# Performance work log

Hardware: AMD Instinct MI355X
Metric: run time of the kernel (lower is better)

The kernel has to match this reference:

```python
import jax, jax.numpy as jnp
import numpy as np

N, E, G = 100000, 600000, 2000
CONV = [128, 256, 256, 256]
LIN = [256, 128, 1]
BN_EPS = 1e-5


def setup_inputs() -> dict:
    key = jax.random.key(0)
    ks = iter(jax.random.split(key, 64))
    inp = {}
    inp["x"] = jax.random.normal(next(ks), (N, CONV[0]), dtype=jnp.float32)
    inp["edge_index"] = jax.random.randint(next(ks), (2, E), 0, N)
    inp["batch"] = jnp.sort(jax.random.randint(next(ks), (N,), 0, G))

    def lin_w(k, i, o):
        return (jax.random.normal(k, (i, o), dtype=jnp.float32) / np.sqrt(i)).astype(jnp.float32)

    # 3 GINConv MLPs: Linear(in,out), BN(out), ReLU, Linear(out,out), ReLU
    for i in range(3):
        ci, co = CONV[i], CONV[i + 1]
        inp[f"c{i}_w1"] = lin_w(next(ks), ci, co)
        inp[f"c{i}_b1"] = jnp.zeros((co,), jnp.float32)
        inp[f"c{i}_g"] = jnp.ones((co,), jnp.float32)
        inp[f"c{i}_be"] = jnp.zeros((co,), jnp.float32)
        inp[f"c{i}_m"] = jax.random.normal(next(ks), (co,), dtype=jnp.float32) * 0.1
        inp[f"c{i}_v"] = jax.random.uniform(next(ks), (co,), minval=0.5, maxval=1.5, dtype=jnp.float32)
        inp[f"c{i}_w2"] = lin_w(next(ks), co, co)
        inp[f"c{i}_b2"] = jnp.zeros((co,), jnp.float32)
    # head: Linear(256,128) + BN(128) + ReLU, Linear(128,1)
    inp["l0_w"] = lin_w(next(ks), LIN[0], LIN[1])
    inp["l0_b"] = jnp.zeros((LIN[1],), jnp.float32)
    inp["l0_g"] = jnp.ones((LIN[1],), jnp.float32)
    inp["l0_be"] = jnp.zeros((LIN[1],), jnp.float32)
    inp["l0_m"] = jax.random.normal(next(ks), (LIN[1],), dtype=jnp.float32) * 0.1
    inp["l0_v"] = jax.random.uniform(next(ks), (LIN[1],), minval=0.5, maxval=1.5, dtype=jnp.float32)
    inp["l1_w"] = lin_w(next(ks), LIN[1], LIN[2])
    inp["l1_b"] = jnp.zeros((LIN[2],), jnp.float32)
    return inp


def _bn(h, g, be, m, v):
    return g * (h - m) * jax.lax.rsqrt(v + BN_EPS) + be


def _gin_conv(x, src, dst, w1, b1, g, be, m, v, w2, b2):
    # GINConv (eps=0): MLP(x + sum_{j in N(i)} x_j); messages x[src] aggregated at dst
    agg = jax.ops.segment_sum(x[src], dst, num_segments=x.shape[0])
    h = (x + agg) @ w1 + b1
    h = jax.nn.relu(_bn(h, g, be, m, v))
    return jax.nn.relu(h @ w2 + b2)


def reference(x, edge_index, batch,
              c0_w1, c0_b1, c0_g, c0_be, c0_m, c0_v, c0_w2, c0_b2,
              c1_w1, c1_b1, c1_g, c1_be, c1_m, c1_v, c1_w2, c1_b2,
              c2_w1, c2_b1, c2_g, c2_be, c2_m, c2_v, c2_w2, c2_b2,
              l0_w, l0_b, l0_g, l0_be, l0_m, l0_v, l1_w, l1_b):
    src, dst = edge_index[0], edge_index[1]
    conv_params = [
        (c0_w1, c0_b1, c0_g, c0_be, c0_m, c0_v, c0_w2, c0_b2),
        (c1_w1, c1_b1, c1_g, c1_be, c1_m, c1_v, c1_w2, c1_b2),
        (c2_w1, c2_b1, c2_g, c2_be, c2_m, c2_v, c2_w2, c2_b2),
    ]
    h = x
    for i, p in enumerate(conv_params):
        h = _gin_conv(h, src, dst, *p)
        if i < 2:
            h = jax.nn.relu(h)  # outer activation (no-op after ReLU, kept for fidelity)
    # global_add_pool over graphs
    h = jax.ops.segment_sum(h, batch, num_segments=G)  # [G, 256]
    h = h @ l0_w + l0_b
    h = _bn(h, l0_g, l0_be, l0_m, l0_v)
    h = jax.nn.relu(h)  # dropout is identity in eval mode
    return h @ l1_w + l1_b  # [G, 1]
```

## Files before the change

kernel.cpp:

```cpp
#include <hip/hip_runtime.h>
#include <hip/hip_bf16.h>

#define BN_EPS 1e-5f

typedef __attribute__((ext_vector_type(8))) short short8;
typedef __attribute__((ext_vector_type(4))) float f32x4;

__device__ __forceinline__ void gll16(const void* g, void* l) {
    __builtin_amdgcn_global_load_lds(
        (const __attribute__((address_space(1))) unsigned int*)g,
        (__attribute__((address_space(3))) unsigned int*)l, 16, 0, 0);
}

__device__ __forceinline__ unsigned pack_bf2(float a, float b) {
    __hip_bfloat16 ba = __float2bfloat16(a);
    __hip_bfloat16 bb = __float2bfloat16(b);
    return (unsigned)(*(unsigned short*)&ba) | ((unsigned)(*(unsigned short*)&bb) << 16);
}

__global__ void hist_kernel(const int* __restrict__ dst, int* __restrict__ off, int E) {
    int e = blockIdx.x * blockDim.x + threadIdx.x;
    if (e < E) atomicAdd(&off[dst[e] + 1], 1);
}

__global__ __launch_bounds__(256) void scan1_kernel(int* __restrict__ data,
                                                    int* __restrict__ sums, int n) {
    __shared__ int sh[256];
    const int t = threadIdx.x;
    const int idx = blockIdx.x * 1024 + t * 4;
    int v[4];
    int s = 0;
#pragma unroll
    for (int j = 0; j < 4; ++j) {
        int x = (idx + j < n) ? data[idx + j] : 0;
        s += x;
        v[j] = s;
    }
    sh[t] = s;
    __syncthreads();
    for (int o = 1; o < 256; o <<= 1) {
        int x = (t >= o) ? sh[t - o] : 0;
        __syncthreads();
        sh[t] += x;
        __syncthreads();
    }
    const int prev = sh[t] - s;
#pragma unroll
    for (int j = 0; j < 4; ++j) {
        if (idx + j < n) data[idx + j] = v[j] + prev;
    }
    if (t == 255) sums[blockIdx.x] = sh[255];
}

__global__ __launch_bounds__(256) void scan2_kernel(int* __restrict__ sums, int nb) {
    __shared__ int sh[256];
    const int t = threadIdx.x;
    sh[t] = (t < nb) ? sums[t] : 0;
    __syncthreads();
    for (int o = 1; o < 256; o <<= 1) {
        int x = (t >= o) ? sh[t - o] : 0;
        __syncthreads();
        sh[t] += x;
        __syncthreads();
    }
    if (t < nb) sums[t] = sh[t];
}

__global__ void scan3_kernel(int* __restrict__ data, const int* __restrict__ sums,
                             int* __restrict__ cursor, int n, int N) {
    int i = blockIdx.x * blockDim.x + threadIdx.x;
    if (i >= n) return;
    int b = i >> 10;
    int v = data[i];
    if (b > 0) { v += sums[b - 1]; data[i] = v; }
    if (i < N) cursor[i] = v;
}

__global__ void fill_kernel(const int* __restrict__ src, const int* __restrict__ dst,
                            int* __restrict__ cursor, int* __restrict__ sorted_src, int E) {
    int e = blockIdx.x * blockDim.x + threadIdx.x;
    if (e >= E) return;
    int p = atomicAdd(&cursor[dst[e]], 1);
    sorted_src[p] = src[e];
}

__global__ void cvt_x_kernel(const float* __restrict__ x, __hip_bfloat16* __restrict__ xb,
                             int N, int total ) {
    int i = blockIdx.x * blockDim.x + threadIdx.x;
    if (i >= total) return;
    int n = i >> 7;
    float v = (n < N) ? x[i] : 0.f;
    xb[i] = __float2bfloat16(v);
}

__global__ void wt_all_kernel(const float* __restrict__ w0, const float* __restrict__ w1,
                              const float* __restrict__ w2, const float* __restrict__ w3,
                              const float* __restrict__ w4, const float* __restrict__ w5,
                              __hip_bfloat16* __restrict__ o0, __hip_bfloat16* __restrict__ o1,
                              __hip_bfloat16* __restrict__ o2, __hip_bfloat16* __restrict__ o3,
                              __hip_bfloat16* __restrict__ o4, __hip_bfloat16* __restrict__ o5) {
    int i = blockIdx.x * blockDim.x + threadIdx.x;
    const int S0 = 256 * 128, S = 256 * 256;
    if (i < S0) {
        int m = i / 128, k = i - m * 128;
        o0[i] = __float2bfloat16(w0[k * 256 + m]);
        return;
    }
    i -= S0;
    int mi = i / S, j = i - mi * S;
    if (mi >= 5) return;
    int m = j >> 8, k = j & 255;
    const float* Wp; __hip_bfloat16* Op;
    switch (mi) {
        case 0: Wp = w1; Op = o1; break;
        case 1: Wp = w2; Op = o2; break;
        case 2: Wp = w3; Op = o3; break;
        case 3: Wp = w4; Op = o4; break;
        default: Wp = w5; Op = o5; break;
    }
    Op[j] = __float2bfloat16(Wp[k * 256 + m]);
}

__global__ void prep_ss_kernel(
    const float* __restrict__ g0, const float* __restrict__ be0, const float* __restrict__ m0,
    const float* __restrict__ v0, const float* __restrict__ b10, const float* __restrict__ b20,
    const float* __restrict__ g1, const float* __restrict__ be1, const float* __restrict__ m1,
    const float* __restrict__ v1, const float* __restrict__ b11, const float* __restrict__ b21,
    const float* __restrict__ g2, const float* __restrict__ be2, const float* __restrict__ m2,
    const float* __restrict__ v2, const float* __restrict__ b12, const float* __restrict__ b22,
    float* __restrict__ ss) {
    const int layer = blockIdx.x;
    const int c = threadIdx.x;
    const float *g, *be, *m, *v, *b1, *b2;
    switch (layer) {
        case 0: g = g0; be = be0; m = m0; v = v0; b1 = b10; b2 = b20; break;
        case 1: g = g1; be = be1; m = m1; v = v1; b1 = b11; b2 = b21; break;
        default: g = g2; be = be2; m = m2; v = v2; b1 = b12; b2 = b22; break;
    }
    float r = rsqrtf(v[c] + BN_EPS);
    float s = g[c] * r;
    ss[(2 * layer) * 512 + c] = s;
    ss[(2 * layer) * 512 + 256 + c] = (b1[c] - m[c]) * s + be[c];
    ss[(2 * layer + 1) * 512 + c] = 1.f;
    ss[(2 * layer + 1) * 512 + 256 + c] = b2[c];
}

template <int C>
__global__ __launch_bounds__(256) void agg_fused(const __hip_bfloat16* __restrict__ h,
                                                 const int* __restrict__ off,
                                                 const int* __restrict__ ssrc,
                                                 __hip_bfloat16* __restrict__ out, int N) {
    constexpr int L = C / 8;
    int t = blockIdx.x * blockDim.x + threadIdx.x;
    int n = t / L;
    if (n >= N) return;
    int c8 = t - n * L;
    const uint4* hp = (const uint4*)h;

    float acc[8];
    {
        uint4 sv = hp[(size_t)n * L + c8];
        const unsigned u[4] = {sv.x, sv.y, sv.z, sv.w};
#pragma unroll
        for (int j = 0; j < 4; ++j) {
            acc[2 * j]     = __uint_as_float(u[j] << 16);
            acc[2 * j + 1] = __uint_as_float(u[j] & 0xffff0000u);
        }
    }
    const int e0 = off[n], e1 = off[n + 1];
    int e = e0;
    for (; e + 2 <= e1; e += 2) {
        int s0 = ssrc[e], s1 = ssrc[e + 1];
        uint4 a = hp[(size_t)s0 * L + c8];
        uint4 b = hp[(size_t)s1 * L + c8];
        const unsigned ua[4] = {a.x, a.y, a.z, a.w};
        const unsigned ub[4] = {b.x, b.y, b.z, b.w};
#pragma unroll
        for (int j = 0; j < 4; ++j) {
            acc[2 * j]     += __uint_as_float(ua[j] << 16);
            acc[2 * j + 1] += __uint_as_float(ua[j] & 0xffff0000u);
            acc[2 * j]     += __uint_as_float(ub[j] << 16);
            acc[2 * j + 1] += __uint_as_float(ub[j] & 0xffff0000u);
        }
    }
    if (e < e1) {
        int s0 = ssrc[e];
        uint4 a = hp[(size_t)s0 * L + c8];
        const unsigned ua[4] = {a.x, a.y, a.z, a.w};
#pragma unroll
        for (int j = 0; j < 4; ++j) {
            acc[2 * j]     += __uint_as_float(ua[j] << 16);
            acc[2 * j + 1] += __uint_as_float(ua[j] & 0xffff0000u);
        }
    }
    unsigned o[4];
#pragma unroll
    for (int j = 0; j < 4; ++j) o[j] = pack_bf2(acc[2 * j], acc[2 * j + 1]);
    ((uint4*)out)[(size_t)n * L + c8] = make_uint4(o[0], o[1], o[2], o[3]);
}

template <int K1>
__global__ __launch_bounds__(512) void mlp_fused(
    const __hip_bfloat16* __restrict__ A,
    const __hip_bfloat16* __restrict__ W1t,
    const __hip_bfloat16* __restrict__ W2t,
    const float* __restrict__ ss1, const float* __restrict__ ss2,
    __hip_bfloat16* __restrict__ C) {
    __shared__ __align__(16) char bufAT[64 * 1024];
    __shared__ __align__(16) char bufW[2][32 * 1024];

    const int tid = threadIdx.x;
    const int l   = tid & 63;
    const int w   = tid >> 6;
    const int wr  = w >> 2;
    const int wc  = w & 3;
    const size_t row0 = (size_t)blockIdx.x * 128;

    constexpr int ROWB = K1 * 2;
    constexpr int NT1  = K1 / 64;
    constexpr int NIA  = 128 * ROWB / 1024;
    constexpr int RPI  = 1024 / ROWB;

    const int lswz = (l & 7) << 4;

    {
        const char* Ab = (const char*)(A + row0 * K1);
#pragma unroll
        for (int i = w; i < NIA; i += 8) {
            int row = i * RPI + (l * 16) / ROWB;
            int byt = ((l * 16) % ROWB) ^ ((row & 7) << 4);
            gll16(Ab + (size_t)row * ROWB + byt, bufAT + i * 1024);
        }
    }
    auto stageW = [&](const __hip_bfloat16* Wsrc, int Krow2, int t, int buf) {
        const char* Wb = (const char*)Wsrc;
#pragma unroll
        for (int i = w; i < 32; i += 8) {
            int c = i * 8 + (l >> 3);
            int byt = ((l & 7) * 16) ^ ((c & 7) << 4);
            gll16(Wb + (size_t)c * Krow2 + t * 128 + byt, bufW[buf] + i * 1024);
        }
    };
    stageW(W1t, ROWB, 0, 0);
    __syncthreads();

    f32x4 acc1[4][4] = {};
    int buf = 0;
#pragma unroll
    for (int t = 0; t < NT1; ++t) {
        if (t + 1 < NT1) stageW(W1t, ROWB, t + 1, buf ^ 1);
        else             stageW(W2t, 512, 0, buf ^ 1);
#pragma unroll
        for (int k0 = 0; k0 < 2; ++k0) {
            short8 wf[4], af[4];
            const int wbyt = (k0 * 64 + (l >> 4) * 16) ^ lswz;
            const int abyt = (t * 128 + k0 * 64 + (l >> 4) * 16) ^ lswz;
#pragma unroll
            for (int i = 0; i < 4; ++i) {
                const int c = wc * 64 + i * 16 + (l & 15);
                wf[i] = *(const short8*)(bufW[buf] + c * 128 + wbyt);
                const int r = wr * 64 + i * 16 + (l & 15);
                af[i] = *(const short8*)(bufAT + r * ROWB + abyt);
            }
#pragma unroll
            for (int mi = 0; mi < 4; ++mi)
#pragma unroll
                for (int nj = 0; nj < 4; ++nj)
                    acc1[mi][nj] = __builtin_amdgcn_mfma_f32_16x16x32_bf16(
                        wf[mi], af[nj], acc1[mi][nj], 0, 0, 0);
        }
        __syncthreads();
        buf ^= 1;
    }

#pragma unroll
    for (int mi = 0; mi < 4; ++mi) {
        const int m0 = wc * 64 + mi * 16 + (l >> 4) * 4;
        const float4 s4 = *(const float4*)(ss1 + m0);
        const float4 h4 = *(const float4*)(ss1 + 256 + m0);
        const int byt = (m0 * 2) ^ lswz;
#pragma unroll
        for (int nj = 0; nj < 4; ++nj) {
            const int n = wr * 64 + nj * 16 + (l & 15);
            const float v0 = fmaxf(acc1[mi][nj][0] * s4.x + h4.x, 0.f);
            const float v1 = fmaxf(acc1[mi][nj][1] * s4.y + h4.y, 0.f);
            const float v2 = fmaxf(acc1[mi][nj][2] * s4.z + h4.z, 0.f);
            const float v3 = fmaxf(acc1[mi][nj][3] * s4.w + h4.w, 0.f);
            *(uint2*)(bufAT + n * 512 + byt) = make_uint2(pack_bf2(v0, v1), pack_bf2(v2, v3));
        }
    }
    __syncthreads();

    f32x4 acc2[4][4] = {};
#pragma unroll
    for (int s = 0; s < 4; ++s) {
        if (s < 3) stageW(W2t, 512, s + 1, buf ^ 1);
#pragma unroll
        for (int k0 = 0; k0 < 2; ++k0) {
            short8 tf[4], wf[4];
            const int tbyt = (s * 128 + k0 * 64 + (l >> 4) * 16) ^ lswz;
            const int wbyt = (k0 * 64 + (l >> 4) * 16) ^ lswz;
#pragma unroll
            for (int i = 0; i < 4; ++i) {
                const int r = wr * 64 + i * 16 + (l & 15);
                tf[i] = *(const short8*)(bufAT + r * 512 + tbyt);
                const int c = wc * 64 + i * 16 + (l & 15);
                wf[i] = *(const short8*)(bufW[buf] + c * 128 + wbyt);
            }
#pragma unroll
            for (int mi = 0; mi < 4; ++mi)
#pragma unroll
                for (int ni = 0; ni < 4; ++ni)
                    acc2[mi][ni] = __builtin_amdgcn_mfma_f32_16x16x32_bf16(
                        tf[mi], wf[ni], acc2[mi][ni], 0, 0, 0);
        }
        if (s < 3) { __syncthreads(); buf ^= 1; }
    }

#pragma unroll
    for (int ni = 0; ni < 4; ++ni) {
        const int col = wc * 64 + ni * 16 + (l & 15);
        const float sc = ss2[col], sh = ss2[256 + col];
#pragma unroll
        for (int mi = 0; mi < 4; ++mi) {
            const size_t grow = row0 + wr * 64 + mi * 16 + (l >> 4) * 4;
#pragma unroll
            for (int r = 0; r < 4; ++r) {
                float vv = fmaxf(acc2[mi][ni][r] * sc + sh, 0.f);
                C[(grow + r) * 256 + col] = __float2bfloat16(vv);
            }
        }
    }
}

__device__ __forceinline__ int lower_bound_dev(const int* __restrict__ a, int n, int key) {
    int lo = 0, hi = n;
    while (lo < hi) {
        int mid = (lo + hi) >> 1;
        if (a[mid] < key) lo = mid + 1; else hi = mid;
    }
    return lo;
}

__global__ __launch_bounds__(256) void pool_seg_kernel(const __hip_bfloat16* __restrict__ h,
                                                       const int* __restrict__ batch,
                                                       float* __restrict__ pooled, int N) {
    __shared__ int seg[2];
    const int g = blockIdx.x;
    if (threadIdx.x == 0) seg[0] = lower_bound_dev(batch, N, g);
    if (threadIdx.x == 1) seg[1] = lower_bound_dev(batch, N, g + 1);
    __syncthreads();
    const int c = threadIdx.x;
    float acc = 0.f;
    for (int n = seg[0]; n < seg[1]; ++n) acc += __bfloat162float(h[(size_t)n * 256 + c]);
    pooled[(size_t)g * 256 + c] = acc;
}

__global__ __launch_bounds__(128) void head_kernel(
    const float* __restrict__ pooled,
    const float* __restrict__ w0, const float* __restrict__ b0,
    const float* __restrict__ g, const float* __restrict__ be,
    const float* __restrict__ m, const float* __restrict__ v,
    const float* __restrict__ w1, const float* __restrict__ b1,
    float* __restrict__ out) {
    __shared__ float row[256];
    __shared__ float red[128];
    const int gid = blockIdx.x;
    const int j = threadIdx.x;

    row[j]       = pooled[(size_t)gid * 256 + j];
    row[j + 128] = pooled[(size_t)gid * 256 + 128 + j];
    __syncthreads();

    float acc = b0[j];
#pragma unroll 8
    for (int k = 0; k < 256; ++k) acc += row[k] * w0[k * 128 + j];

    float h = g[j] * (acc - m[j]) * rsqrtf(v[j] + BN_EPS) + be[j];
    h = fmaxf(h, 0.f) * w1[j];
    red[j] = h;
    __syncthreads();
    for (int s = 64; s > 0; s >>= 1) {
        if (j < s) red[j] += red[j + s];
        __syncthreads();
    }
    if (j == 0) out[gid] = red[0] + b1[0];
}

extern "C" void kernel_launch(void* const* d_in, const int* in_sizes, int n_in,
                              void* d_out, int out_size, void* d_ws, size_t ws_size,
                              hipStream_t stream) {
    const float* x    = (const float*)d_in[0];
    const int* eidx   = (const int*)d_in[1];
    const int* batch  = (const int*)d_in[2];

    const int N = in_sizes[0] / 128;
    const int E = in_sizes[1] / 2;
    const int G = out_size;

    const int* src = eidx;
    const int* dst = eidx + E;

    const float* cw1[3]; const float* cb1[3]; const float* cg[3]; const float* cbe[3];
    const float* cm[3];  const float* cv[3];  const float* cw2[3]; const float* cb2[3];
    for (int i = 0; i < 3; ++i) {
        int b = 3 + i * 8;
        cw1[i] = (const float*)d_in[b + 0];
        cb1[i] = (const float*)d_in[b + 1];
        cg[i]  = (const float*)d_in[b + 2];
        cbe[i] = (const float*)d_in[b + 3];
        cm[i]  = (const float*)d_in[b + 4];
        cv[i]  = (const float*)d_in[b + 5];
        cw2[i] = (const float*)d_in[b + 6];
        cb2[i] = (const float*)d_in[b + 7];
    }
    const float* l0_w  = (const float*)d_in[27];
    const float* l0_b  = (const float*)d_in[28];
    const float* l0_g  = (const float*)d_in[29];
    const float* l0_be = (const float*)d_in[30];
    const float* l0_m  = (const float*)d_in[31];
    const float* l0_v  = (const float*)d_in[32];
    const float* l1_w  = (const float*)d_in[33];
    const float* l1_b  = (const float*)d_in[34];

    float* outp = (float*)d_out;

    const int nrb  = (N + 127) / 128;
    const int Npad = nrb * 128;
    const size_t SB = (size_t)Npad * 256 * 2;
    const size_t XB = (size_t)Npad * 128 * 2;
    const size_t PB = (size_t)G * 256 * 4;
    const size_t WTB = (size_t)256 * 256 * 2;

    char* ws = (char*)d_ws;
    size_t o = 0;
    __hip_bfloat16* U  = (__hip_bfloat16*)(ws + o); o += SB;
    __hip_bfloat16* V  = (__hip_bfloat16*)(ws + o); o += SB;
    __hip_bfloat16* xb = (__hip_bfloat16*)(ws + o); o += XB;
    float* pooled      = (float*)(ws + o);       o += PB;
    __hip_bfloat16* wt[6];
    for (int i = 0; i < 6; ++i) { wt[i] = (__hip_bfloat16*)(ws + o); o += WTB; }
    float* ss          = (float*)(ws + o);       o += 6 * 512 * 4;
    int* csr_off    = (int*)(ws + o); o += (size_t)(N + 1) * 4;
    int* cursor     = (int*)(ws + o); o += (size_t)N * 4;
    int* sorted_src = (int*)(ws + o); o += (size_t)E * 4;
    int* sums       = (int*)(ws + o); o += 256 * 4;
    if (ws_size < o) return;

    const dim3 blk(256);

    {
        int total = Npad * 128;
        cvt_x_kernel<<<(total + 255) / 256, blk, 0, stream>>>(x, xb, N, total);
    }
    {
        int total = 256 * 128 + 5 * 256 * 256;
        wt_all_kernel<<<(total + 255) / 256, blk, 0, stream>>>(
            cw1[0], cw2[0], cw1[1], cw2[1], cw1[2], cw2[2],
            wt[0], wt[1], wt[2], wt[3], wt[4], wt[5]);
    }
    prep_ss_kernel<<<3, blk, 0, stream>>>(
        cg[0], cbe[0], cm[0], cv[0], cb1[0], cb2[0],
        cg[1], cbe[1], cm[1], cv[1], cb1[1], cb2[1],
        cg[2], cbe[2], cm[2], cv[2], cb1[2], cb2[2], ss);

    {
        const int n_off = N + 1;
        hipMemsetAsync(csr_off, 0, (size_t)n_off * sizeof(int), stream);
        hist_kernel<<<(E + 255) / 256, blk, 0, stream>>>(dst, csr_off, E);
        const int nb = (n_off + 1023) / 1024;
        scan1_kernel<<<nb, blk, 0, stream>>>(csr_off, sums, n_off);
        scan2_kernel<<<1, blk, 0, stream>>>(sums, nb);
        scan3_kernel<<<(n_off + 255) / 256, blk, 0, stream>>>(csr_off, sums, cursor, n_off, N);
        fill_kernel<<<(E + 255) / 256, blk, 0, stream>>>(src, dst, cursor, sorted_src, E);
    }

    auto SS = [&](int i) { return ss + i * 512; };

    {
        int total = N * 16;
        agg_fused<128><<<(total + 255) / 256, blk, 0, stream>>>(xb, csr_off, sorted_src, U, N);
    }
    mlp_fused<128><<<nrb, dim3(512), 0, stream>>>(U, wt[0], wt[1], SS(0), SS(1), V);

    {
        int total = N * 32;
        agg_fused<256><<<(total + 255) / 256, blk, 0, stream>>>(V, csr_off, sorted_src, U, N);
    }
    mlp_fused<256><<<nrb, dim3(512), 0, stream>>>(U, wt[2], wt[3], SS(2), SS(3), U);

    {
        int total = N * 32;
        agg_fused<256><<<(total + 255) / 256, blk, 0, stream>>>(U, csr_off, sorted_src, V, N);
    }
    mlp_fused<256><<<nrb, dim3(512), 0, stream>>>(V, wt[4], wt[5], SS(4), SS(5), V);

    pool_seg_kernel<<<G, blk, 0, stream>>>(V, batch, pooled, N);
    head_kernel<<<G, dim3(128), 0, stream>>>(pooled, l0_w, l0_b, l0_g, l0_be, l0_m, l0_v,
                                             l1_w, l1_b, outp);
}
```

Baseline: 437.1 us.

## Halve MLP row tile, single-buffer weights, and stage output through LDS

The fused MLP kernel now handles 64 rows per block instead of 128 and cuts LDS from 128 KB to 64 KB by dropping the double-buffered weight tiles. It also halves the accumulator count and sets a launch bound of 4 blocks per CU, all aimed at higher occupancy. The output is written through LDS and stored as coalesced 16-byte rows instead of scattered 2-byte stores. In exchange, weight loads are no longer overlapped with MFMA work, each block waits on vmcnt and adds barriers, and every weight tile is re-read from memory by twice as many blocks.

```diff
diff --git a/kernel.cpp b/kernel.cpp
--- a/kernel.cpp
+++ b/kernel.cpp
@@ -200,31 +200,30 @@
 }
 
 template <int K1>
-__global__ __launch_bounds__(512) void mlp_fused(
+__global__ __launch_bounds__(512, 4) void mlp_fused(
     const __hip_bfloat16* __restrict__ A,
     const __hip_bfloat16* __restrict__ W1t,
     const __hip_bfloat16* __restrict__ W2t,
     const float* __restrict__ ss1, const float* __restrict__ ss2,
     __hip_bfloat16* __restrict__ C) {
-    __shared__ __align__(16) char bufAT[64 * 1024];
-    __shared__ __align__(16) char bufW[2][32 * 1024];
+    __shared__ __align__(16) char bufAT[32 * 1024];
+    __shared__ __align__(16) char bufW[32 * 1024];
 
     const int tid = threadIdx.x;
     const int l   = tid & 63;
     const int w   = tid >> 6;
     const int wr  = w >> 2;
     const int wc  = w & 3;
-    const size_t row0 = (size_t)blockIdx.x * 128;
+    const size_t row0 = (size_t)blockIdx.x * 64;
 
     constexpr int ROWB = K1 * 2;
     constexpr int NT1  = K1 / 64;
-    constexpr int NIA  = 128 * ROWB / 1024;
-    constexpr int RPI  = 1024 / ROWB;
-
     const int lswz = (l & 7) << 4;
 
     {
         const char* Ab = (const char*)(A + row0 * K1);
+        constexpr int NIA = 64 * ROWB / 1024;
+        constexpr int RPI = 1024 / ROWB;
 #pragma unroll
         for (int i = w; i < NIA; i += 8) {
             int row = i * RPI + (l * 16) / ROWB;
@@ -232,47 +231,48 @@
             gll16(Ab + (size_t)row * ROWB + byt, bufAT + i * 1024);
         }
     }
-    auto stageW = [&](const __hip_bfloat16* Wsrc, int Krow2, int t, int buf) {
-        const char* Wb = (const char*)Wsrc;
+    auto stageW = [&](const __hip_bfloat16* Wsrc, int Krow2, int t) {
 #pragma unroll
         for (int i = w; i < 32; i += 8) {
             int c = i * 8 + (l >> 3);
-            int byt = ((l & 7) * 16) ^ ((c & 7) << 4);
-            gll16(Wb + (size_t)c * Krow2 + t * 128 + byt, bufW[buf] + i * 1024);
+            int byt = ((l & 7) * 16) ^ ((l >> 3) << 4);
+            gll16((const char*)Wsrc + (size_t)c * Krow2 + t * 128 + byt, bufW + i * 1024);
         }
     };
-    stageW(W1t, ROWB, 0, 0);
-    __syncthreads();
-
-    f32x4 acc1[4][4] = {};
-    int buf = 0;
+    stageW(W1t, ROWB, 0);
+    asm volatile("s_waitcnt vmcnt(0)" ::: "memory");
+    __syncthreads();
+
+    f32x4 acc1[4][2] = {};
 #pragma unroll
     for (int t = 0; t < NT1; ++t) {
-        if (t + 1 < NT1) stageW(W1t, ROWB, t + 1, buf ^ 1);
-        else             stageW(W2t, 512, 0, buf ^ 1);
 #pragma unroll
         for (int k0 = 0; k0 < 2; ++k0) {
-            short8 wf[4], af[4];
+            short8 wf[4], af[2];
             const int wbyt = (k0 * 64 + (l >> 4) * 16) ^ lswz;
             const int abyt = (t * 128 + k0 * 64 + (l >> 4) * 16) ^ lswz;
 #pragma unroll
-            for (int i = 0; i < 4; ++i) {
-                const int c = wc * 64 + i * 16 + (l & 15);
-                wf[i] = *(const short8*)(bufW[buf] + c * 128 + wbyt);
-                const int r = wr * 64 + i * 16 + (l & 15);
-                af[i] = *(const short8*)(bufAT + r * ROWB + abyt);
-            }
+            for (int i = 0; i < 4; ++i)
+                wf[i] = *(const short8*)(bufW + (wc * 64 + i * 16 + (l & 15)) * 128 + wbyt);
+#pragma unroll
+            for (int i = 0; i < 2; ++i)
+                af[i] = *(const short8*)(bufAT + (wr * 32 + i * 16 + (l & 15)) * ROWB + abyt);
 #pragma unroll
             for (int mi = 0; mi < 4; ++mi)
 #pragma unroll
-                for (int nj = 0; nj < 4; ++nj)
+                for (int nj = 0; nj < 2; ++nj)
                     acc1[mi][nj] = __builtin_amdgcn_mfma_f32_16x16x32_bf16(
                         wf[mi], af[nj], acc1[mi][nj], 0, 0, 0);
         }
         __syncthreads();
-        buf ^= 1;
-    }
-
+        if (t + 1 < NT1) {
+            stageW(W1t, ROWB, t + 1);
+            asm volatile("s_waitcnt vmcnt(0)" ::: "memory");
+            __syncthreads();
+        }
+    }
+
+    stageW(W2t, 512, 0);
 #pragma unroll
     for (int mi = 0; mi < 4; ++mi) {
         const int m0 = wc * 64 + mi * 16 + (l >> 4) * 4;
@@ -280,8 +280,8 @@
         const float4 h4 = *(const float4*)(ss1 + 256 + m0);
         const int byt = (m0 * 2) ^ lswz;
 #pragma unroll
-        for (int nj = 0; nj < 4; ++nj) {
-            const int n = wr * 64 + nj * 16 + (l & 15);
+        for (int nj = 0; nj < 2; ++nj) {
+            const int n = wr * 32 + nj * 16 + (l & 15);
             const float v0 = fmaxf(acc1[mi][nj][0] * s4.x + h4.x, 0.f);
             const float v1 = fmaxf(acc1[mi][nj][1] * s4.y + h4.y, 0.f);
             const float v2 = fmaxf(acc1[mi][nj][2] * s4.z + h4.z, 0.f);
@@ -289,46 +289,64 @@
             *(uint2*)(bufAT + n * 512 + byt) = make_uint2(pack_bf2(v0, v1), pack_bf2(v2, v3));
         }
     }
-    __syncthreads();
-
-    f32x4 acc2[4][4] = {};
+    asm volatile("s_waitcnt vmcnt(0)" ::: "memory");
+    __syncthreads();
+
+    f32x4 acc2[4][2] = {};
 #pragma unroll
     for (int s = 0; s < 4; ++s) {
-        if (s < 3) stageW(W2t, 512, s + 1, buf ^ 1);
 #pragma unroll
         for (int k0 = 0; k0 < 2; ++k0) {
-            short8 tf[4], wf[4];
+            short8 wf[4], tf[2];
+            const int wbyt = (k0 * 64 + (l >> 4) * 16) ^ lswz;
             const int tbyt = (s * 128 + k0 * 64 + (l >> 4) * 16) ^ lswz;
-            const int wbyt = (k0 * 64 + (l >> 4) * 16) ^ lswz;
-#pragma unroll
-            for (int i = 0; i < 4; ++i) {
-                const int r = wr * 64 + i * 16 + (l & 15);
-                tf[i] = *(const short8*)(bufAT + r * 512 + tbyt);
-                const int c = wc * 64 + i * 16 + (l & 15);
-                wf[i] = *(const short8*)(bufW[buf] + c * 128 + wbyt);
-            }
-#pragma unroll
-            for (int mi = 0; mi < 4; ++mi)
-#pragma unroll
-                for (int ni = 0; ni < 4; ++ni)
-                    acc2[mi][ni] = __builtin_amdgcn_mfma_f32_16x16x32_bf16(
-                        tf[mi], wf[ni], acc2[mi][ni], 0, 0, 0);
-        }
-        if (s < 3) { __syncthreads(); buf ^= 1; }
+#pragma unroll
+            for (int i = 0; i < 4; ++i)
+                wf[i] = *(const short8*)(bufW + (wc * 64 + i * 16 + (l & 15)) * 128 + wbyt);
+#pragma unroll
+            for (int i = 0; i < 2; ++i)
+                tf[i] = *(const short8*)(bufAT + (wr * 32 + i * 16 + (l & 15)) * 512 + tbyt);
+#pragma unroll
+            for (int ni = 0; ni < 4; ++ni)
+#pragma unroll
+                for (int mj = 0; mj < 2; ++mj)
+                    acc2[ni][mj] = __builtin_amdgcn_mfma_f32_16x16x32_bf16(
+                        wf[ni], tf[mj], acc2[ni][mj], 0, 0, 0);
+        }
+        __syncthreads();
+        if (s < 3) {
+            stageW(W2t, 512, s + 1);
+            asm volatile("s_waitcnt vmcnt(0)" ::: "memory");
+            __syncthreads();
+        }
     }
 
 #pragma unroll
     for (int ni = 0; ni < 4; ++ni) {
-        const int col = wc * 64 + ni * 16 + (l & 15);
-        const float sc = ss2[col], sh = ss2[256 + col];
-#pragma unroll
-        for (int mi = 0; mi < 4; ++mi) {
-            const size_t grow = row0 + wr * 64 + mi * 16 + (l >> 4) * 4;
-#pragma unroll
-            for (int r = 0; r < 4; ++r) {
-                float vv = fmaxf(acc2[mi][ni][r] * sc + sh, 0.f);
-                C[(grow + r) * 256 + col] = __float2bfloat16(vv);
-            }
+        const int c0 = wc * 64 + ni * 16 + (l >> 4) * 4;
+        const float4 s4 = *(const float4*)(ss2 + c0);
+        const float4 h4 = *(const float4*)(ss2 + 256 + c0);
+        const int byt = (c0 * 2) ^ lswz;
+#pragma unroll
+        for (int mj = 0; mj < 2; ++mj) {
+            const int n = wr * 32 + mj * 16 + (l & 15);
+            const float v0 = fmaxf(acc2[ni][mj][0] * s4.x + h4.x, 0.f);
+            const float v1 = fmaxf(acc2[ni][mj][1] * s4.y + h4.y, 0.f);
+            const float v2 = fmaxf(acc2[ni][mj][2] * s4.z + h4.z, 0.f);
+            const float v3 = fmaxf(acc2[ni][mj][3] * s4.w + h4.w, 0.f);
+            *(uint2*)(bufAT + n * 512 + byt) = make_uint2(pack_bf2(v0, v1), pack_bf2(v2, v3));
+        }
+    }
+    __syncthreads();
+
+    {
+        char* Cb = (char*)C + row0 * 512;
+#pragma unroll
+        for (int q = tid; q < 2048; q += 512) {
+            const int n = q >> 5;
+            const int slot = (q & 31) * 16;
+            uint4 v = *(const uint4*)(bufAT + n * 512 + (slot ^ ((n & 7) << 4)));
+            *(uint4*)(Cb + q * 16) = v;
         }
     }
 }
@@ -427,6 +445,7 @@
 
     const int nrb  = (N + 127) / 128;
     const int Npad = nrb * 128;
+    const int nrb64 = Npad / 64;
     const size_t SB = (size_t)Npad * 256 * 2;
     const size_t XB = (size_t)Npad * 128 * 2;
     const size_t PB = (size_t)G * 256 * 4;
@@ -481,19 +500,19 @@
         int total = N * 16;
         agg_fused<128><<<(total + 255) / 256, blk, 0, stream>>>(xb, csr_off, sorted_src, U, N);
     }
-    mlp_fused<128><<<nrb, dim3(512), 0, stream>>>(U, wt[0], wt[1], SS(0), SS(1), V);
+    mlp_fused<128><<<nrb64, dim3(512), 0, stream>>>(U, wt[0], wt[1], SS(0), SS(1), V);
 
     {
         int total = N * 32;
         agg_fused<256><<<(total + 255) / 256, blk, 0, stream>>>(V, csr_off, sorted_src, U, N);
     }
-    mlp_fused<256><<<nrb, dim3(512), 0, stream>>>(U, wt[2], wt[3], SS(2), SS(3), U);
+    mlp_fused<256><<<nrb64, dim3(512), 0, stream>>>(U, wt[2], wt[3], SS(2), SS(3), U);
 
     {
         int total = N * 32;
         agg_fused<256><<<(total + 255) / 256, blk, 0, stream>>>(U, csr_off, sorted_src, V, N);
     }
-    mlp_fused<256><<<nrb, dim3(512), 0, stream>>>(V, wt[4], wt[5], SS(4), SS(5), V);
+    mlp_fused<256><<<nrb64, dim3(512), 0, stream>>>(V, wt[4], wt[5], SS(4), SS(5), V);
 
     pool_seg_kernel<<<G, blk, 0, stream>>>(V, batch, pooled, N);
     head_kernel<<<G, dim3(128), 0, stream>>>(pooled, l0_w, l0_b, l0_g, l0_be, l0_m, l0_v,
```

After: 405.5 us. -7.2%, faster.
